# Kernel tuning notes

Hardware: AMD Instinct MI355X
Metric: run time of the kernel (lower is better)

The kernel has to match this reference:

```python
import jax, jax.numpy as jnp
import numpy as np

N = 32768      # total nodes
B = 64         # graphs
NPG = 512      # nodes per graph
E = 524288     # edges (avg degree 16)
H = 4          # heads
Fh = 64        # per-head dim
C = H * Fh     # 256
FIN = 128
RATIO = 0.5


def gat(x, src, dst, W, a_src, a_dst, bias, n_nodes):
    # PyG GATConv: linear -> add self-loops -> edge softmax over dst -> scatter-add
    h = (x @ W).reshape(n_nodes, H, Fh)
    loop = jnp.arange(n_nodes)
    s = jnp.concatenate([src, loop])
    d = jnp.concatenate([dst, loop])
    es = jnp.sum(h * a_src, axis=-1)  # [N,H]
    ed = jnp.sum(h * a_dst, axis=-1)  # [N,H]
    e = jax.nn.leaky_relu(es[s] + ed[d], 0.2)  # [E+N,H]
    m = jax.ops.segment_max(e, d, num_segments=n_nodes)
    ex = jnp.exp(e - m[d])
    den = jax.ops.segment_sum(ex, d, num_segments=n_nodes)
    alpha = ex / (den[d] + 1e-16)  # [E+N,H]
    out = jax.ops.segment_sum(alpha[:, :, None] * h[s], d, num_segments=n_nodes)
    return out.reshape(n_nodes, C) + bias


def pool(x, sw, sb, tw, tb, n_graphs, n_per):
    # equal-size graphs -> per-graph top-k as a batched top_k
    k = max(1, int(n_per * RATIO))
    scores = jax.nn.sigmoid(x @ sw + sb)[:, 0].reshape(n_graphs, n_per)
    _, idx = jax.lax.top_k(scores, k)  # [B,k]
    xb = x.reshape(n_graphs, n_per, x.shape[-1])
    sel = jnp.take_along_axis(xb, idx[:, :, None], axis=1)
    sel = sel.reshape(n_graphs * k, x.shape[-1])
    return sel @ tw + tb, k


def setup_inputs() -> dict:
    key = jax.random.key(0)
    ks = jax.random.split(key, 24)
    x = jax.random.normal(ks[0], (N, FIN), dtype=jnp.float32)
    # within-graph random edges
    gbase = jnp.repeat(jnp.arange(B, dtype=jnp.int32) * NPG, E // B)
    src = gbase + jax.random.randint(ks[1], (E,), 0, NPG)
    dst = gbase + jax.random.randint(ks[2], (E,), 0, NPG)
    edge_index = jnp.stack([src, dst]).astype(jnp.int32)
    batch = jnp.repeat(jnp.arange(B, dtype=jnp.int32), NPG)
    def lin(k, fi, fo):
        return jax.random.normal(k, (fi, fo), dtype=jnp.float32) / np.sqrt(fi)
    inp = dict(x=x, edge_index=edge_index, batch=batch)
    inp["W1"] = lin(ks[3], FIN, C)
    inp["a_src1"] = jax.random.normal(ks[4], (H, Fh), jnp.float32) / np.sqrt(Fh)
    inp["a_dst1"] = jax.random.normal(ks[5], (H, Fh), jnp.float32) / np.sqrt(Fh)
    inp["b1"] = jnp.zeros((C,), jnp.float32)
    inp["W2"] = lin(ks[6], C, C)
    inp["a_src2"] = jax.random.normal(ks[7], (H, Fh), jnp.float32) / np.sqrt(Fh)
    inp["a_dst2"] = jax.random.normal(ks[8], (H, Fh), jnp.float32) / np.sqrt(Fh)
    inp["b2"] = jnp.zeros((C,), jnp.float32)
    inp["p1_sw"] = lin(ks[9], C, 1)
    inp["p1_sb"] = jnp.zeros((1,), jnp.float32)
    inp["p1_tw"] = lin(ks[10], C, C)
    inp["p1_tb"] = jnp.zeros((C,), jnp.float32)
    inp["p2_sw"] = lin(ks[11], C, 1)
    inp["p2_sb"] = jnp.zeros((1,), jnp.float32)
    inp["p2_tw"] = lin(ks[12], C, C)
    inp["p2_tb"] = jnp.zeros((C,), jnp.float32)
    inp["c1w"] = lin(ks[13], C, 64)
    inp["c1b"] = jnp.zeros((64,), jnp.float32)
    inp["c2w"] = lin(ks[14], 64, 2)
    inp["c2b"] = jnp.zeros((2,), jnp.float32)
    return inp


def reference(x, edge_index, batch, W1, a_src1, a_dst1, b1, W2, a_src2, a_dst2, b2,
              p1_sw, p1_sb, p1_tw, p1_tb, p2_sw, p2_sb, p2_tw, p2_tb,
              c1w, c1b, c2w, c2b):
    src, dst = edge_index[0], edge_index[1]
    h = jax.nn.elu(gat(x, src, dst, W1, a_src1, a_dst1, b1, N))
    h = jax.nn.elu(gat(h, src, dst, W2, a_src2, a_dst2, b2, N))
    # pool1 then pool2 (edge_index after pooling is never consumed by the output path)
    h, k1 = pool(h, p1_sw, p1_sb, p1_tw, p1_tb, B, NPG)
    h, k2 = pool(h, p2_sw, p2_sb, p2_tw, p2_tb, B, k1)
    g = h.reshape(B, k2, C).mean(axis=1)  # global mean pool per graph
    g = jax.nn.relu(g @ c1w + c1b)
    g = g @ c2w + c2b
    return jax.nn.log_softmax(g, axis=1)
```

## Files before the change

kernel.cpp:

```cpp
#include <hip/hip_runtime.h>
#include <hip/hip_bf16.h>
#include <hip/hip_fp16.h>
#include <math.h>

constexpr int NN  = 32768;
constexpr int BG  = 64;
constexpr int NPG = 512;
constexpr int EG  = 524288;
constexpr int EPG = EG / BG;
constexpr int HH  = 4;
constexpr int FH  = 64;
constexpr int CC  = 256;
constexpr int FIN = 128;
constexpr int KP1 = 256;
constexpr int KP2 = 128;
constexpr int NS  = 4;

typedef __attribute__((ext_vector_type(8))) short short8;
typedef __attribute__((ext_vector_type(4))) float f32x4;
typedef __attribute__((ext_vector_type(2))) float f32x2v;

__device__ inline float leaky02(float v) { return v > 0.0f ? v : 0.2f * v; }

__device__ inline unsigned short f2bf(float v) {
    __hip_bfloat16 h = __float2bfloat16(v);
    return *(unsigned short*)&h;
}
__device__ inline float bf2f(unsigned short u) {
    __hip_bfloat16 h;
    *(unsigned short*)&h = u;
    return __bfloat162float(h);
}
__device__ inline void split2(float v, unsigned short& hi, unsigned short& lo) {
    hi = f2bf(v);
    lo = f2bf(v - bf2f(hi));
}
__device__ inline void split8(const float* p, short8& hi, short8& lo) {
    const float4 f0 = *(const float4*)p;
    const float4 f1 = *(const float4*)(p + 4);
    unsigned short h, l;
    split2(f0.x, h, l); hi[0] = (short)h; lo[0] = (short)l;
    split2(f0.y, h, l); hi[1] = (short)h; lo[1] = (short)l;
    split2(f0.z, h, l); hi[2] = (short)h; lo[2] = (short)l;
    split2(f0.w, h, l); hi[3] = (short)h; lo[3] = (short)l;
    split2(f1.x, h, l); hi[4] = (short)h; lo[4] = (short)l;
    split2(f1.y, h, l); hi[5] = (short)h; lo[5] = (short)l;
    split2(f1.z, h, l); hi[6] = (short)h; lo[6] = (short)l;
    split2(f1.w, h, l); hi[7] = (short)h; lo[7] = (short)l;
}

__device__ inline unsigned short f2h(float v) {
    __half h = __float2half(v);
    return *(unsigned short*)&h;
}

__device__ inline unsigned int fmap(float v) {
    unsigned int b = __float_as_uint(v);
    return (b & 0x80000000u) ? ~b : (b | 0x80000000u);
}

__device__ inline void acc8h(const unsigned short* p, float a, f32x2v* acc) {
    const uint4 u = *(const uint4*)p;
    const __half2* hp = (const __half2*)&u;
    f32x2v av; av[0] = a; av[1] = a;
#pragma unroll
    for (int i = 0; i < 4; ++i) {
        const float2 f = __half22float2(hp[i]);
        f32x2v fv; fv[0] = f.x; fv[1] = f.y;
        acc[i] = __builtin_elementwise_fma(fv, av, acc[i]);
    }
}

__global__ __launch_bounds__(1024) void setup_k(
        const int* __restrict__ src, const int* __restrict__ dst,
        int* __restrict__ rowp, int* __restrict__ esrc,
        const float* __restrict__ tw1, const float* __restrict__ sw2,
        const float* __restrict__ tb1, const float* __restrict__ sb2,
        float* __restrict__ w12, float* __restrict__ b12,
        const float* __restrict__ tw2, const float* __restrict__ c1w,
        const float* __restrict__ tb2, float* __restrict__ T,
        float* __restrict__ bc2,
        const float* __restrict__ W1, const float* __restrict__ W2,
        unsigned short* __restrict__ w1ph, unsigned short* __restrict__ w1pl,
        unsigned short* __restrict__ w2ph, unsigned short* __restrict__ w2pl) {
    __shared__ int lcnt[NPG];
    __shared__ int wsum[8];
    const int b = blockIdx.x;
    const int t = threadIdx.x;
    if (b < BG) {
        const int g = b;
        const int ebase = g * EPG;
        const int nbase = g * NPG;
        if (t < NPG) lcnt[t] = 0;
        __syncthreads();
        int ds[EPG / 1024];
#pragma unroll
        for (int j = 0; j < EPG / 1024; ++j) {
            ds[j] = dst[ebase + t + 1024 * j] - nbase;
            atomicAdd(&lcnt[ds[j]], 1);
        }
        __syncthreads();
        int c = 0, sInc = 0;
        if (t < NPG) {
            c = lcnt[t];
            sInc = c;
#pragma unroll
            for (int o = 1; o < 64; o <<= 1) {
                int v = __shfl_up(sInc, o);
                if ((t & 63) >= o) sInc += v;
            }
            if ((t & 63) == 63) wsum[t >> 6] = sInc;
        }
        __syncthreads();
        if (t < 8) {
            int v = wsum[t];
            int s = v;
#pragma unroll
            for (int o = 1; o < 8; o <<= 1) {
                int u2 = __shfl_up(s, o, 8);
                if (t >= o) s += u2;
            }
            wsum[t] = s - v;
        }
        __syncthreads();
        if (t < NPG) {
            const int ex = sInc - c + wsum[t >> 6];
            rowp[nbase + t] = ebase + ex;
            lcnt[t] = ex;
        }
        if (g == BG - 1 && t == 0) rowp[NN] = EG;
        __syncthreads();
#pragma unroll
        for (int j = 0; j < EPG / 1024; ++j) {
            int p = atomicAdd(&lcnt[ds[j]], 1);
            esrc[ebase + p] = src[ebase + t + 1024 * j];
        }
        return;
    }
    if (t >= 256) return;
    const int pb = b - BG;
    if (pb < 66) {
        if (pb == 0) {
            float s = 0.0f;
            for (int o = 0; o < CC; ++o) s += tw1[t * CC + o] * sw2[o];
            w12[t] = s;
            if (t == 0) {
                float bb = 0.0f;
                for (int o = 0; o < CC; ++o) bb += tb1[o] * sw2[o];
                *b12 = bb + sb2[0];
            }
        } else if (pb < 65) {
            const int r = (pb - 1) * 4 + (t >> 6);
            const int cth = t & 63;
            float s = 0.0f;
            for (int j = 0; j < CC; ++j) s = fmaf(tw2[r * CC + j], c1w[j * 64 + cth], s);
            T[r * 64 + cth] = s;
        } else if (t < 64) {
            float s = 0.0f;
            for (int j = 0; j < CC; ++j) s = fmaf(tb2[j], c1w[j * 64 + t], s);
            bc2[t] = s;
        }
    } else {
        const int idx = (pb - 66) * 256 + t;
        if (idx < 4096) {
            const int nt = idx >> 8, rem = idx & 255;
            const int kg = rem >> 6, l = rem & 63;
            const int n = nt * 16 + (l & 15);
            const int kb = kg * 32 + (l >> 4) * 8;
            unsigned short h[8], lo[8];
#pragma unroll
            for (int j = 0; j < 8; ++j) split2(W1[(kb + j) * CC + n], h[j], lo[j]);
#pragma unroll
            for (int j = 0; j < 8; ++j) {
                w1ph[(size_t)idx * 8 + j] = h[j];
                w1pl[(size_t)idx * 8 + j] = lo[j];
            }
        } else {
            const int i2 = idx - 4096;
            const int nt = i2 >> 9, rem = i2 & 511;
            const int kg = rem >> 6, l = rem & 63;
            const int n = nt * 16 + (l & 15);
            const int kb = kg * 32 + (l >> 4) * 8;
            unsigned short h[8], lo[8];
#pragma unroll
            for (int j = 0; j < 8; ++j) split2(W2[(kb + j) * CC + n], h[j], lo[j]);
#pragma unroll
            for (int j = 0; j < 8; ++j) {
                w2ph[(size_t)i2 * 8 + j] = h[j];
                w2pl[(size_t)i2 * 8 + j] = lo[j];
            }
        }
    }
}

__global__ __launch_bounds__(256, 4) void gemm_mfma_attn(
        const unsigned short* __restrict__ Ahi, const unsigned short* __restrict__ Alo,
        const unsigned short* __restrict__ Bph, const unsigned short* __restrict__ Bpl,
        unsigned short* __restrict__ Cb, int K,
        const float* __restrict__ a_src, const float* __restrict__ a_dst,
        float* __restrict__ es, float* __restrict__ ed) {
    const int t = threadIdx.x;
    const int w = t >> 6;
    const int l = t & 63;
    const int bx   = blockIdx.x;
    const int xcd  = bx & 7;
    const int slot = bx >> 3;
    const int gph  = xcd + ((slot >> 4) << 3);
    const int row0 = gph * NPG + ((slot & 15) << 5);
    const int m = l & 15;
    const int q = l >> 4;
    const int ncol0 = w * 64;
    const int KG = K >> 5;

    const unsigned short* aH0 = Ahi + (size_t)(row0 + m) * K + q * 8;
    const unsigned short* aL0 = Alo + (size_t)(row0 + m) * K + q * 8;
    const unsigned short* aH1 = aH0 + (size_t)16 * K;
    const unsigned short* aL1 = aL0 + (size_t)16 * K;

    f32x4 acc0[4], acc1[4];
#pragma unroll
    for (int c = 0; c < 4; ++c) {
        acc0[c] = (f32x4){0.f, 0.f, 0.f, 0.f};
        acc1[c] = (f32x4){0.f, 0.f, 0.f, 0.f};
    }

    for (int kg = 0; kg < KG; ++kg) {
        const int ko = kg * 32;
        short8 ah0 = *(const short8*)(aH0 + ko);
        short8 al0 = *(const short8*)(aL0 + ko);
        short8 ah1 = *(const short8*)(aH1 + ko);
        short8 al1 = *(const short8*)(aL1 + ko);
#pragma unroll
        for (int c = 0; c < 4; ++c) {
            const int nt = (w << 2) + c;
            const size_t boff = ((size_t)(nt * KG + kg) * 64 + l) * 8;
            short8 bh = *(const short8*)(Bph + boff);
            short8 bl = *(const short8*)(Bpl + boff);
            acc0[c] = __builtin_amdgcn_mfma_f32_16x16x32_bf16(ah0, bh, acc0[c], 0, 0, 0);
            acc0[c] = __builtin_amdgcn_mfma_f32_16x16x32_bf16(ah0, bl, acc0[c], 0, 0, 0);
            acc0[c] = __builtin_amdgcn_mfma_f32_16x16x32_bf16(al0, bh, acc0[c], 0, 0, 0);
            acc1[c] = __builtin_amdgcn_mfma_f32_16x16x32_bf16(ah1, bh, acc1[c], 0, 0, 0);
            acc1[c] = __builtin_amdgcn_mfma_f32_16x16x32_bf16(ah1, bl, acc1[c], 0, 0, 0);
            acc1[c] = __builtin_amdgcn_mfma_f32_16x16x32_bf16(al1, bh, acc1[c], 0, 0, 0);
        }
    }

#pragma unroll
    for (int c = 0; c < 4; ++c)
#pragma unroll
        for (int r = 0; r < 4; ++r) {
            Cb[(size_t)(row0 + q * 4 + r) * CC + ncol0 + c * 16 + m] = f2h(acc0[c][r]);
            Cb[(size_t)(row0 + 16 + q * 4 + r) * CC + ncol0 + c * 16 + m] = f2h(acc1[c][r]);
        }

    float asv[4], adv[4];
#pragma unroll
    for (int c = 0; c < 4; ++c) {
        asv[c] = a_src[ncol0 + c * 16 + m];
        adv[c] = a_dst[ncol0 + c * 16 + m];
    }
#pragma unroll
    for (int r = 0; r < 4; ++r) {
        float ps0 = 0.f, pd0 = 0.f, ps1 = 0.f, pd1 = 0.f;
#pragma unroll
        for (int c = 0; c < 4; ++c) {
            ps0 = fmaf(acc0[c][r], asv[c], ps0);
            pd0 = fmaf(acc0[c][r], adv[c], pd0);
            ps1 = fmaf(acc1[c][r], asv[c], ps1);
            pd1 = fmaf(acc1[c][r], adv[c], pd1);
        }
#pragma unroll
        for (int o = 8; o >= 1; o >>= 1) {
            ps0 += __shfl_down(ps0, o, 16);
            pd0 += __shfl_down(pd0, o, 16);
            ps1 += __shfl_down(ps1, o, 16);
            pd1 += __shfl_down(pd1, o, 16);
        }
        if (m == 0) {
            es[(row0 + q * 4 + r) * HH + w] = ps0;
            ed[(row0 + q * 4 + r) * HH + w] = pd0;
            es[(row0 + 16 + q * 4 + r) * HH + w] = ps1;
            ed[(row0 + 16 + q * 4 + r) * HH + w] = pd1;
        }
    }
}

__global__ __launch_bounds__(256, 4) void gemm_mfma_attn_f32(
        const float* __restrict__ Af,
        const unsigned short* __restrict__ Bph, const unsigned short* __restrict__ Bpl,
        unsigned short* __restrict__ Cb, int K,
        const float* __restrict__ a_src, const float* __restrict__ a_dst,
        float* __restrict__ es, float* __restrict__ ed,
        const float* __restrict__ tw1, const float* __restrict__ T,
        const float* __restrict__ tb1, const float* __restrict__ bc2,
        const float* __restrict__ c1b, float* __restrict__ Wc,
        float* __restrict__ bcv) {
    const int t = threadIdx.x;
    const int bx = blockIdx.x;
    if (bx >= NN / 32) {
        const int fb = bx - NN / 32;
        if (fb < 64) {
            const int r = fb * 4 + (t >> 6);
            const int cth = t & 63;
            float s = 0.0f;
            for (int j = 0; j < CC; ++j) s = fmaf(tw1[r * CC + j], T[j * 64 + cth], s);
            Wc[r * 64 + cth] = s;
        } else if (t < 64) {
            float s = 0.0f;
            for (int j = 0; j < CC; ++j) s = fmaf(tb1[j], T[j * 64 + t], s);
            bcv[t] = s + bc2[t] + c1b[t];
        }
        return;
    }
    const int w = t >> 6;
    const int l = t & 63;
    const int xcd  = bx & 7;
    const int slot = bx >> 3;
    const int gph  = xcd + ((slot >> 4) << 3);
    const int row0 = gph * NPG + ((slot & 15) << 5);
    const int m = l & 15;
    const int q = l >> 4;
    const int ncol0 = w * 64;
    const int KG = K >> 5;

    const float* aF0 = Af + (size_t)(row0 + m) * K + q * 8;
    const float* aF1 = aF0 + (size_t)16 * K;

    f32x4 acc0[4], acc1[4];
#pragma unroll
    for (int c = 0; c < 4; ++c) {
        acc0[c] = (f32x4){0.f, 0.f, 0.f, 0.f};
        acc1[c] = (f32x4){0.f, 0.f, 0.f, 0.f};
    }

    for (int kg = 0; kg < KG; ++kg) {
        const int ko = kg * 32;
        short8 ah0, al0, ah1, al1;
        split8(aF0 + ko, ah0, al0);
        split8(aF1 + ko, ah1, al1);
#pragma unroll
        for (int c = 0; c < 4; ++c) {
            const int nt = (w << 2) + c;
            const size_t boff = ((size_t)(nt * KG + kg) * 64 + l) * 8;
            short8 bh = *(const short8*)(Bph + boff);
            short8 bl = *(const short8*)(Bpl + boff);
            acc0[c] = __builtin_amdgcn_mfma_f32_16x16x32_bf16(ah0, bh, acc0[c], 0, 0, 0);
            acc0[c] = __builtin_amdgcn_mfma_f32_16x16x32_bf16(ah0, bl, acc0[c], 0, 0, 0);
            acc0[c] = __builtin_amdgcn_mfma_f32_16x16x32_bf16(al0, bh, acc0[c], 0, 0, 0);
            acc1[c] = __builtin_amdgcn_mfma_f32_16x16x32_bf16(ah1, bh, acc1[c], 0, 0, 0);
            acc1[c] = __builtin_amdgcn_mfma_f32_16x16x32_bf16(ah1, bl, acc1[c], 0, 0, 0);
            acc1[c] = __builtin_amdgcn_mfma_f32_16x16x32_bf16(al1, bh, acc1[c], 0, 0, 0);
        }
    }

#pragma unroll
    for (int c = 0; c < 4; ++c)
#pragma unroll
        for (int r = 0; r < 4; ++r) {
            Cb[(size_t)(row0 + q * 4 + r) * CC + ncol0 + c * 16 + m] = f2h(acc0[c][r]);
            Cb[(size_t)(row0 + 16 + q * 4 + r) * CC + ncol0 + c * 16 + m] = f2h(acc1[c][r]);
        }

    float asv[4], adv[4];
#pragma unroll
    for (int c = 0; c < 4; ++c) {
        asv[c] = a_src[ncol0 + c * 16 + m];
        adv[c] = a_dst[ncol0 + c * 16 + m];
    }
#pragma unroll
    for (int r = 0; r < 4; ++r) {
        float ps0 = 0.f, pd0 = 0.f, ps1 = 0.f, pd1 = 0.f;
#pragma unroll
        for (int c = 0; c < 4; ++c) {
            ps0 = fmaf(acc0[c][r], asv[c], ps0);
            pd0 = fmaf(acc0[c][r], adv[c], pd0);
            ps1 = fmaf(acc1[c][r], asv[c], ps1);
            pd1 = fmaf(acc1[c][r], adv[c], pd1);
        }
#pragma unroll
        for (int o = 8; o >= 1; o >>= 1) {
            ps0 += __shfl_down(ps0, o, 16);
            pd0 += __shfl_down(pd0, o, 16);
            ps1 += __shfl_down(ps1, o, 16);
            pd1 += __shfl_down(pd1, o, 16);
        }
        if (m == 0) {
            es[(row0 + q * 4 + r) * HH + w] = ps0;
            ed[(row0 + q * 4 + r) * HH + w] = pd0;
            es[(row0 + 16 + q * 4 + r) * HH + w] = ps1;
            ed[(row0 + 16 + q * 4 + r) * HH + w] = pd1;
        }
    }
}

__global__ __launch_bounds__(256) void gat_edge(const unsigned short* __restrict__ zh,
                                                const int* __restrict__ rowp,
                                                const int* __restrict__ esrc,
                                                const float* __restrict__ es,
                                                const float* __restrict__ ed,
                                                const float* __restrict__ bias,
                                                float* __restrict__ out,
                                                unsigned short* __restrict__ outh,
                                                unsigned short* __restrict__ outl,
                                                const float* __restrict__ sw1,
                                                const float* __restrict__ sb1,
                                                const float* __restrict__ w12,
                                                const float* __restrict__ b12,
                                                float* __restrict__ sc1,
                                                float* __restrict__ sc2) {
    const int w = threadIdx.x >> 6;
    const int l = threadIdx.x & 63;
    const int b    = blockIdx.x;
    const int xcd  = b & 7;
    const int slot = b >> 3;
    const int gph  = xcd + ((slot >> 7) << 3);
    const int d    = gph * NPG + ((slot & 127) << 2) + w;

    const int h    = l & 3;
    const int ei   = l >> 2;
    const int lh   = l & 31;
    const int half = l >> 5;
    const int hcol = lh >> 3;
    const int c0   = lh << 3;

    const int beg = rowp[d];
    const int deg = rowp[d + 1] - beg;

    f32x2v acc[4];
#pragma unroll
    for (int i = 0; i < 4; ++i) acc[i] = (f32x2v){0.f, 0.f};

    if (deg <= 16 * NS) {
        const float edh = ed[d * HH + h];
        int   sidx[NS];
        float v[NS];
#pragma unroll
        for (int j = 0; j < NS; ++j) { sidx[j] = d; v[j] = 0.0f; }
        float vmax = -INFINITY, eself = 0.0f, vself = 0.0f;
        if (ei == 0) {
            vself = leaky02(es[d * HH + h] + edh);
            vmax = vself;
        }
#pragma unroll
        for (int j = 0; j < NS; ++j) {
            int i = ei + 16 * j;
            if (i < deg) {
                sidx[j] = esrc[beg + i];
                v[j] = leaky02(es[sidx[j] * HH + h] + edh);
                vmax = fmaxf(vmax, v[j]);
            }
        }
#pragma unroll
        for (int o = 4; o <= 32; o <<= 1) vmax = fmaxf(vmax, __shfl_xor(vmax, o));
        float dsum = 0.0f;
#pragma unroll
        for (int j = 0; j < NS; ++j) {
            int i = ei + 16 * j;
            if (i < deg) { v[j] = __expf(v[j] - vmax); dsum += v[j]; }
        }
        if (ei == 0) { eself = __expf(vself - vmax); dsum += eself; }
#pragma unroll
        for (int o = 4; o <= 32; o <<= 1) dsum += __shfl_xor(dsum, o);
        const float inv = 1.0f / (dsum + 1e-16f);
#pragma unroll
        for (int j = 0; j < NS; ++j) v[j] *= inv;
        eself *= inv;

        float aself = __shfl(eself, hcol);
        if (half) aself = 0.0f;
        acc8h(zh + (size_t)d * CC + c0, aself, acc);

#pragma unroll
        for (int j = 0; j < NS; ++j) {
            if (16 * j < deg) {
#pragma unroll
                for (int rr = 0; rr < 8; ++rr) {
                    if (16 * j + 2 * rr < deg) {
                        const int slb  = (2 * rr + half) << 2;
                        const int srcn = __shfl(sidx[j], slb);
                        const float a  = __shfl(v[j], slb + hcol);
                        acc8h(zh + (size_t)srcn * CC + c0, a, acc);
                    }
                }
            }
        }
    } else {
        const float edh = ed[d * HH + h];
        float vmax = (ei == 0) ? leaky02(es[d * HH + h] + edh) : -INFINITY;
        for (int i = ei; i < deg; i += 16)
            vmax = fmaxf(vmax, leaky02(es[esrc[beg + i] * HH + h] + edh));
#pragma unroll
        for (int o = 4; o <= 32; o <<= 1) vmax = fmaxf(vmax, __shfl_xor(vmax, o));
        float dsum = (ei == 0) ? __expf(leaky02(es[d * HH + h] + edh) - vmax) : 0.0f;
        for (int i = ei; i < deg; i += 16)
            dsum += __expf(leaky02(es[esrc[beg + i] * HH + h] + edh) - vmax);
#pragma unroll
        for (int o = 4; o <= 32; o <<= 1) dsum += __shfl_xor(dsum, o);
        const float inv = 1.0f / (dsum + 1e-16f);

        const float vmaxc = __shfl(vmax, hcol);
        const float invc  = __shfl(inv,  hcol);
        const float edh4  = ed[d * HH + hcol];
        float a0 = __expf(leaky02(es[d * HH + hcol] + edh4) - vmaxc) * invc;
        if (half) a0 = 0.0f;
        acc8h(zh + (size_t)d * CC + c0, a0, acc);
        for (int e = half; e < deg; e += 2) {
            const int srcn = esrc[beg + e];
            const float a = __expf(leaky02(es[srcn * HH + hcol] + edh4) - vmaxc) * invc;
            acc8h(zh + (size_t)srcn * CC + c0, a, acc);
        }
    }

#pragma unroll
    for (int i = 0; i < 4; ++i) {
        float a0 = acc[i][0]; a0 += __shfl_xor(a0, 32);
        float a1 = acc[i][1]; a1 += __shfl_xor(a1, 32);
        acc[i][0] = a0; acc[i][1] = a1;
    }

    const int cw = c0 + (half << 2);
    float o0 = half ? acc[2][0] : acc[0][0];
    float o1 = half ? acc[2][1] : acc[0][1];
    float o2 = half ? acc[3][0] : acc[1][0];
    float o3 = half ? acc[3][1] : acc[1][1];

    const float4 bv = *(const float4*)(bias + cw);
    o0 += bv.x; o0 = o0 > 0.0f ? o0 : __expf(o0) - 1.0f;
    o1 += bv.y; o1 = o1 > 0.0f ? o1 : __expf(o1) - 1.0f;
    o2 += bv.z; o2 = o2 > 0.0f ? o2 : __expf(o2) - 1.0f;
    o3 += bv.w; o3 = o3 > 0.0f ? o3 : __expf(o3) - 1.0f;

    if (out) *(float4*)(out + (size_t)d * CC + cw) = make_float4(o0, o1, o2, o3);
    if (outh) {
        ushort4 uh, ul;
        split2(o0, uh.x, ul.x);
        split2(o1, uh.y, ul.y);
        split2(o2, uh.z, ul.z);
        split2(o3, uh.w, ul.w);
        *(ushort4*)(outh + (size_t)d * CC + cw) = uh;
        *(ushort4*)(outl + (size_t)d * CC + cw) = ul;
    }

    if (sc1) {
        const float4 s1 = *(const float4*)(sw1 + cw);
        const float4 s2 = *(const float4*)(w12 + cw);
        float r1 = o0 * s1.x + o1 * s1.y + o2 * s1.z + o3 * s1.w;
        float r2 = o0 * s2.x + o1 * s2.y + o2 * s2.z + o3 * s2.w;
#pragma unroll
        for (int off = 32; off >= 1; off >>= 1) {
            r1 += __shfl_xor(r1, off);
            r2 += __shfl_xor(r2, off);
        }
        if (l == 0) {
            sc1[d] = r1 + sb1[0];
            sc2[d] = r2 + b12[0];
        }
    }
}

__global__ __launch_bounds__(512) void pool_g(const float* __restrict__ sc1,
                                              const float* __restrict__ sc2,
                                              const float* __restrict__ feat,
                                              const float* __restrict__ Wc,
                                              const float* __restrict__ bc,
                                              const float* __restrict__ c2w,
                                              const float* __restrict__ c2b,
                                              float* __restrict__ outp) {
    __shared__ unsigned int us[NPG];
    __shared__ unsigned char kb[NPG];
    __shared__ int list[KP2];
    __shared__ float v0[CC];
    __shared__ float vbuf[2][CC];
    __shared__ float part[4][64];
    __shared__ float v2[64];
    const int g = blockIdx.x;
    const int t = threadIdx.x;
    const int lane = t & 63, wid = t >> 6;

    const float s2val = sc2[(size_t)g * NPG + t];
    us[t] = fmap(sc1[(size_t)g * NPG + t]);
    __syncthreads();

    if (wid == 0) {
        unsigned int u[8];
#pragma unroll
        for (int j = 0; j < 8; ++j) u[j] = us[j * 64 + lane];
        unsigned int p = 0;
        for (int bb = 31; bb >= 0; --bb) {
            const unsigned int cand = p | (1u << bb);
            int cnt = 0;
#pragma unroll
            for (int j = 0; j < 8; ++j) cnt += __popcll(__ballot(u[j] >= cand));
            if (cnt >= KP1) p = cand;
        }
        int cgt = 0;
#pragma unroll
        for (int j = 0; j < 8; ++j) cgt += __popcll(__ballot(u[j] > p));
        const int kk = KP1 - cgt;
        const unsigned long long lm = (1ull << lane) - 1ull;
        int preEq = 0;
#pragma unroll
        for (int j = 0; j < 8; ++j) {
            const unsigned long long balEq = __ballot(u[j] == p);
            const int eqr = preEq + __popcll(balEq & lm);
            preEq += __popcll(balEq);
            kb[j * 64 + lane] =
                (unsigned char)((u[j] > p) || ((u[j] == p) && (eqr < kk)));
        }
    }
    __syncthreads();

    us[t] = kb[t] ? fmap(s2val) : 0u;
    __syncthreads();
    if (wid == 0) {
        unsigned int u[8];
#pragma unroll
        for (int j = 0; j < 8; ++j) u[j] = us[j * 64 + lane];
        unsigned int p = 0;
        for (int bb = 31; bb >= 0; --bb) {
            const unsigned int cand = p | (1u << bb);
            int cnt = 0;
#pragma unroll
            for (int j = 0; j < 8; ++j) cnt += __popcll(__ballot(u[j] >= cand));
            if (cnt >= KP2) p = cand;
        }
        int cgt = 0;
#pragma unroll
        for (int j = 0; j < 8; ++j) cgt += __popcll(__ballot(u[j] > p));
        const int kk = KP2 - cgt;
        const unsigned long long lm = (1ull << lane) - 1ull;
        int preEq = 0, preKeep = 0;
#pragma unroll
        for (int j = 0; j < 8; ++j) {
            const unsigned long long balEq = __ballot(u[j] == p);
            const int eqr = preEq + __popcll(balEq & lm);
            preEq += __popcll(balEq);
            const int keep = (u[j] > p) || ((u[j] == p) && (eqr < kk));
            const unsigned long long balK = __ballot(keep);
            const int pos = preKeep + __popcll(balK & lm);
            preKeep += __popcll(balK);
            if (keep) list[pos] = j * 64 + lane;
        }
    }
    __syncthreads();

    {
        const int col = t & (CC - 1);
        const int hf = t >> 8;
        float acc = 0.0f;
        for (int i = hf * 64; i < hf * 64 + 64; ++i)
            acc += feat[((size_t)g * NPG + list[i]) * CC + col];
        vbuf[hf][col] = acc;
    }
    __syncthreads();
    if (t < CC) v0[t] = (vbuf[0][t] + vbuf[1][t]) * (1.0f / KP2);
    __syncthreads();

    if (t < 256) {
        const int q = t >> 6, cth = t & 63;
        float pr = 0.0f;
        for (int j = q * 64; j < q * 64 + 64; ++j)
            pr = fmaf(v0[j], Wc[j * 64 + cth], pr);
        part[q][cth] = pr;
    }
    __syncthreads();
    if (t < 64) {
        float u = bc[t];
#pragma unroll
        for (int q = 0; q < 4; ++q) u += part[q][t];
        v2[t] = fmaxf(u, 0.0f);
    }
    __syncthreads();
    if (t < 2) {
        float o = c2b[t];
        for (int j = 0; j < 64; ++j) o = fmaf(v2[j], c2w[j * 2 + t], o);
        part[0][t] = o;
    }
    __syncthreads();
    if (t == 0) {
        float a = part[0][0], bq = part[0][1];
        float mx = fmaxf(a, bq);
        float lse = mx + logf(expf(a - mx) + expf(bq - mx));
        outp[g * 2 + 0] = a - lse;
        outp[g * 2 + 1] = bq - lse;
    }
}

extern "C" void kernel_launch(void* const* d_in, const int* in_sizes, int n_in,
                              void* d_out, int out_size, void* d_ws, size_t ws_size,
                              hipStream_t stream) {
    const float* x      = (const float*)d_in[0];
    const int*   ei     = (const int*)d_in[1];
    const int*   src    = ei;
    const int*   dst    = ei + EG;
    const float* W1     = (const float*)d_in[3];
    const float* a_src1 = (const float*)d_in[4];
    const float* a_dst1 = (const float*)d_in[5];
    const float* b1     = (const float*)d_in[6];
    const float* W2     = (const float*)d_in[7];
    const float* a_src2 = (const float*)d_in[8];
    const float* a_dst2 = (const float*)d_in[9];
    const float* b2     = (const float*)d_in[10];
    const float* p1_sw  = (const float*)d_in[11];
    const float* p1_sb  = (const float*)d_in[12];
    const float* p1_tw  = (const float*)d_in[13];
    const float* p1_tb  = (const float*)d_in[14];
    const float* p2_sw  = (const float*)d_in[15];
    const float* p2_sb  = (const float*)d_in[16];
    const float* p2_tw  = (const float*)d_in[17];
    const float* p2_tb  = (const float*)d_in[18];
    const float* c1w    = (const float*)d_in[19];
    const float* c1b    = (const float*)d_in[20];
    const float* c2w    = (const float*)d_in[21];
    const float* c2b    = (const float*)d_in[22];
    float* out = (float*)d_out;

    float* ws = (float*)d_ws;
    float* z = ws;
    unsigned short* zh = (unsigned short*)z;
    float* fregion = z + (size_t)NN * CC;
    unsigned short* fhi = (unsigned short*)fregion;
    unsigned short* flo = fhi + (size_t)NN * CC;
    float* featF = fregion;
    float* wsp = fregion + (size_t)NN * CC;
    unsigned short* w1ph = (unsigned short*)wsp;
    unsigned short* w1pl = w1ph + 256 * FIN;
    unsigned short* w2ph = w1pl + 256 * FIN;
    unsigned short* w2pl = w2ph + 256 * CC;
    float* es  = (float*)(w2pl + 256 * CC);
    float* ed  = es + NN * HH;
    int* rowp  = (int*)(ed + NN * HH);
    int* esrc  = rowp + NN + 1;
    float* sc1 = (float*)(esrc + EG);
    float* sc2 = sc1 + NN;
    int* sel1  = (int*)(sc2 + NN);
    float* w12 = (float*)(sel1 + NN);
    float* b12 = w12 + CC;
    float* T   = b12 + 64;
    float* Wc  = T + CC * 64;
    float* bc2 = Wc + CC * 64;
    float* bcv = bc2 + 64;

    setup_k<<<BG + 66 + 48, 1024, 0, stream>>>(
        src, dst, rowp, esrc,
        p1_tw, p2_sw, p1_tb, p2_sb, w12, b12, p2_tw, c1w, p2_tb, T, bc2,
        W1, W2, w1ph, w1pl, w2ph, w2pl);

    gemm_mfma_attn_f32<<<NN / 32 + 65, 256, 0, stream>>>(
        x, w1ph, w1pl, zh, FIN, a_src1, a_dst1, es, ed,
        p1_tw, T, p1_tb, bc2, c1b, Wc, bcv);
    gat_edge<<<NN / 4, 256, 0, stream>>>(zh, rowp, esrc, es, ed, b1,
                                         nullptr, fhi, flo,
                                         nullptr, nullptr, nullptr, nullptr,
                                         nullptr, nullptr);

    gemm_mfma_attn<<<NN / 32, 256, 0, stream>>>(fhi, flo, w2ph, w2pl, zh, CC,
                                                a_src2, a_dst2, es, ed);
    gat_edge<<<NN / 4, 256, 0, stream>>>(zh, rowp, esrc, es, ed, b2,
                                         featF, nullptr, nullptr,
                                         p1_sw, p1_sb, w12, b12, sc1, sc2);

    pool_g<<<BG, 512, 0, stream>>>(sc1, sc2, featF, Wc, bcv, c2w, c2b, out);
}
```

Baseline: 258.6 us.

## Fuse first GAT edge aggregation with second-layer GEMM through shared memory

The first-layer edge softmax/aggregation is merged with the second-layer MFMA GEMM into one kernel. Each block aggregates 32 destination rows, stores the split hi/lo bf16 features in swizzled LDS, then runs the GEMM and attention-logit reduction from LDS. This removes the global write and reload of the hi/lo intermediate feature matrices and one kernel launch. In exchange, the edge phase now runs with fewer blocks (32 rows per block instead of 4), which lowers parallelism for the gather. It also uses 32KB of LDS per block and needs separate zh2/es2/ed2 buffers.

Result: faster. 243.4 us (-5.9%).

```diff
diff --git a/kernel.cpp b/kernel.cpp
--- a/kernel.cpp
+++ b/kernel.cpp
@@ -189,98 +189,6 @@
                 w2ph[(size_t)i2 * 8 + j] = h[j];
                 w2pl[(size_t)i2 * 8 + j] = lo[j];
             }
-        }
-    }
-}
-
-__global__ __launch_bounds__(256, 4) void gemm_mfma_attn(
-        const unsigned short* __restrict__ Ahi, const unsigned short* __restrict__ Alo,
-        const unsigned short* __restrict__ Bph, const unsigned short* __restrict__ Bpl,
-        unsigned short* __restrict__ Cb, int K,
-        const float* __restrict__ a_src, const float* __restrict__ a_dst,
-        float* __restrict__ es, float* __restrict__ ed) {
-    const int t = threadIdx.x;
-    const int w = t >> 6;
-    const int l = t & 63;
-    const int bx   = blockIdx.x;
-    const int xcd  = bx & 7;
-    const int slot = bx >> 3;
-    const int gph  = xcd + ((slot >> 4) << 3);
-    const int row0 = gph * NPG + ((slot & 15) << 5);
-    const int m = l & 15;
-    const int q = l >> 4;
-    const int ncol0 = w * 64;
-    const int KG = K >> 5;
-
-    const unsigned short* aH0 = Ahi + (size_t)(row0 + m) * K + q * 8;
-    const unsigned short* aL0 = Alo + (size_t)(row0 + m) * K + q * 8;
-    const unsigned short* aH1 = aH0 + (size_t)16 * K;
-    const unsigned short* aL1 = aL0 + (size_t)16 * K;
-
-    f32x4 acc0[4], acc1[4];
-#pragma unroll
-    for (int c = 0; c < 4; ++c) {
-        acc0[c] = (f32x4){0.f, 0.f, 0.f, 0.f};
-        acc1[c] = (f32x4){0.f, 0.f, 0.f, 0.f};
-    }
-
-    for (int kg = 0; kg < KG; ++kg) {
-        const int ko = kg * 32;
-        short8 ah0 = *(const short8*)(aH0 + ko);
-        short8 al0 = *(const short8*)(aL0 + ko);
-        short8 ah1 = *(const short8*)(aH1 + ko);
-        short8 al1 = *(const short8*)(aL1 + ko);
-#pragma unroll
-        for (int c = 0; c < 4; ++c) {
-            const int nt = (w << 2) + c;
-            const size_t boff = ((size_t)(nt * KG + kg) * 64 + l) * 8;
-            short8 bh = *(const short8*)(Bph + boff);
-            short8 bl = *(const short8*)(Bpl + boff);
-            acc0[c] = __builtin_amdgcn_mfma_f32_16x16x32_bf16(ah0, bh, acc0[c], 0, 0, 0);
-            acc0[c] = __builtin_amdgcn_mfma_f32_16x16x32_bf16(ah0, bl, acc0[c], 0, 0, 0);
-            acc0[c] = __builtin_amdgcn_mfma_f32_16x16x32_bf16(al0, bh, acc0[c], 0, 0, 0);
-            acc1[c] = __builtin_amdgcn_mfma_f32_16x16x32_bf16(ah1, bh, acc1[c], 0, 0, 0);
-            acc1[c] = __builtin_amdgcn_mfma_f32_16x16x32_bf16(ah1, bl, acc1[c], 0, 0, 0);
-            acc1[c] = __builtin_amdgcn_mfma_f32_16x16x32_bf16(al1, bh, acc1[c], 0, 0, 0);
-        }
-    }
-
-#pragma unroll
-    for (int c = 0; c < 4; ++c)
-#pragma unroll
-        for (int r = 0; r < 4; ++r) {
-            Cb[(size_t)(row0 + q * 4 + r) * CC + ncol0 + c * 16 + m] = f2h(acc0[c][r]);
-            Cb[(size_t)(row0 + 16 + q * 4 + r) * CC + ncol0 + c * 16 + m] = f2h(acc1[c][r]);
-        }
-
-    float asv[4], adv[4];
-#pragma unroll
-    for (int c = 0; c < 4; ++c) {
-        asv[c] = a_src[ncol0 + c * 16 + m];
-        adv[c] = a_dst[ncol0 + c * 16 + m];
-    }
-#pragma unroll
-    for (int r = 0; r < 4; ++r) {
-        float ps0 = 0.f, pd0 = 0.f, ps1 = 0.f, pd1 = 0.f;
-#pragma unroll
-        for (int c = 0; c < 4; ++c) {
-            ps0 = fmaf(acc0[c][r], asv[c], ps0);
-            pd0 = fmaf(acc0[c][r], adv[c], pd0);
-            ps1 = fmaf(acc1[c][r], asv[c], ps1);
-            pd1 = fmaf(acc1[c][r], adv[c], pd1);
-        }
-#pragma unroll
-        for (int o = 8; o >= 1; o >>= 1) {
-            ps0 += __shfl_down(ps0, o, 16);
-            pd0 += __shfl_down(pd0, o, 16);
-            ps1 += __shfl_down(ps1, o, 16);
-            pd1 += __shfl_down(pd1, o, 16);
-        }
-        if (m == 0) {
-            es[(row0 + q * 4 + r) * HH + w] = ps0;
-            ed[(row0 + q * 4 + r) * HH + w] = pd0;
-            es[(row0 + 16 + q * 4 + r) * HH + w] = ps1;
-            ed[(row0 + 16 + q * 4 + r) * HH + w] = pd1;
         }
     }
 }
@@ -393,6 +301,230 @@
     }
 }
 
+__global__ __launch_bounds__(256) void edge1_gemm2(
+        const unsigned short* __restrict__ zh1,
+        const int* __restrict__ rowp, const int* __restrict__ esrc,
+        const float* __restrict__ es1, const float* __restrict__ ed1,
+        const float* __restrict__ bias,
+        const unsigned short* __restrict__ Bph, const unsigned short* __restrict__ Bpl,
+        unsigned short* __restrict__ zh2,
+        const float* __restrict__ a_src, const float* __restrict__ a_dst,
+        float* __restrict__ es2, float* __restrict__ ed2) {
+    __shared__ unsigned char AhB[32 * 512];
+    __shared__ unsigned char AlB[32 * 512];
+    const int t = threadIdx.x;
+    const int w = t >> 6;
+    const int l = t & 63;
+    const int bx   = blockIdx.x;
+    const int xcd  = bx & 7;
+    const int slot = bx >> 3;
+    const int gph  = xcd + ((slot >> 4) << 3);
+    const int row0 = gph * NPG + ((slot & 15) << 5);
+
+    const int h    = l & 3;
+    const int ei   = l >> 2;
+    const int lh   = l & 31;
+    const int half = l >> 5;
+    const int hcol = lh >> 3;
+    const int c0   = lh << 3;
+
+    for (int nd = 0; nd < 8; ++nd) {
+        const int rloc = w * 8 + nd;
+        const int d = row0 + rloc;
+        const int beg = rowp[d];
+        const int deg = rowp[d + 1] - beg;
+
+        f32x2v acc[4];
+#pragma unroll
+        for (int i = 0; i < 4; ++i) acc[i] = (f32x2v){0.f, 0.f};
+
+        if (deg <= 16 * NS) {
+            const float edh = ed1[d * HH + h];
+            int   sidx[NS];
+            float v[NS];
+#pragma unroll
+            for (int j = 0; j < NS; ++j) { sidx[j] = d; v[j] = 0.0f; }
+            float vmax = -INFINITY, eself = 0.0f, vself = 0.0f;
+            if (ei == 0) {
+                vself = leaky02(es1[d * HH + h] + edh);
+                vmax = vself;
+            }
+#pragma unroll
+            for (int j = 0; j < NS; ++j) {
+                int i = ei + 16 * j;
+                if (i < deg) {
+                    sidx[j] = esrc[beg + i];
+                    v[j] = leaky02(es1[sidx[j] * HH + h] + edh);
+                    vmax = fmaxf(vmax, v[j]);
+                }
+            }
+#pragma unroll
+            for (int o = 4; o <= 32; o <<= 1) vmax = fmaxf(vmax, __shfl_xor(vmax, o));
+            float dsum = 0.0f;
+#pragma unroll
+            for (int j = 0; j < NS; ++j) {
+                int i = ei + 16 * j;
+                if (i < deg) { v[j] = __expf(v[j] - vmax); dsum += v[j]; }
+            }
+            if (ei == 0) { eself = __expf(vself - vmax); dsum += eself; }
+#pragma unroll
+            for (int o = 4; o <= 32; o <<= 1) dsum += __shfl_xor(dsum, o);
+            const float inv = 1.0f / (dsum + 1e-16f);
+#pragma unroll
+            for (int j = 0; j < NS; ++j) v[j] *= inv;
+            eself *= inv;
+
+            float aself = __shfl(eself, hcol);
+            if (half) aself = 0.0f;
+            acc8h(zh1 + (size_t)d * CC + c0, aself, acc);
+
+#pragma unroll
+            for (int j = 0; j < NS; ++j) {
+                if (16 * j < deg) {
+#pragma unroll
+                    for (int rr = 0; rr < 8; ++rr) {
+                        if (16 * j + 2 * rr < deg) {
+                            const int slb  = (2 * rr + half) << 2;
+                            const int srcn = __shfl(sidx[j], slb);
+                            const float a  = __shfl(v[j], slb + hcol);
+                            acc8h(zh1 + (size_t)srcn * CC + c0, a, acc);
+                        }
+                    }
+                }
+            }
+        } else {
+            const float edh = ed1[d * HH + h];
+            float vmax = (ei == 0) ? leaky02(es1[d * HH + h] + edh) : -INFINITY;
+            for (int i = ei; i < deg; i += 16)
+                vmax = fmaxf(vmax, leaky02(es1[esrc[beg + i] * HH + h] + edh));
+#pragma unroll
+            for (int o = 4; o <= 32; o <<= 1) vmax = fmaxf(vmax, __shfl_xor(vmax, o));
+            float dsum = (ei == 0) ? __expf(leaky02(es1[d * HH + h] + edh) - vmax) : 0.0f;
+            for (int i = ei; i < deg; i += 16)
+                dsum += __expf(leaky02(es1[esrc[beg + i] * HH + h] + edh) - vmax);
+#pragma unroll
+            for (int o = 4; o <= 32; o <<= 1) dsum += __shfl_xor(dsum, o);
+            const float inv = 1.0f / (dsum + 1e-16f);
+
+            const float vmaxc = __shfl(vmax, hcol);
+            const float invc  = __shfl(inv,  hcol);
+            const float edh4  = ed1[d * HH + hcol];
+            float a0 = __expf(leaky02(es1[d * HH + hcol] + edh4) - vmaxc) * invc;
+            if (half) a0 = 0.0f;
+            acc8h(zh1 + (size_t)d * CC + c0, a0, acc);
+            for (int e = half; e < deg; e += 2) {
+                const int srcn = esrc[beg + e];
+                const float a = __expf(leaky02(es1[srcn * HH + hcol] + edh4) - vmaxc) * invc;
+                acc8h(zh1 + (size_t)srcn * CC + c0, a, acc);
+            }
+        }
+
+#pragma unroll
+        for (int i = 0; i < 4; ++i) {
+            float a0 = acc[i][0]; a0 += __shfl_xor(a0, 32);
+            float a1 = acc[i][1]; a1 += __shfl_xor(a1, 32);
+            acc[i][0] = a0; acc[i][1] = a1;
+        }
+
+        const int cw = c0 + (half << 2);
+        float o0 = half ? acc[2][0] : acc[0][0];
+        float o1 = half ? acc[2][1] : acc[0][1];
+        float o2 = half ? acc[3][0] : acc[1][0];
+        float o3 = half ? acc[3][1] : acc[1][1];
+
+        const float4 bv = *(const float4*)(bias + cw);
+        o0 += bv.x; o0 = o0 > 0.0f ? o0 : __expf(o0) - 1.0f;
+        o1 += bv.y; o1 = o1 > 0.0f ? o1 : __expf(o1) - 1.0f;
+        o2 += bv.z; o2 = o2 > 0.0f ? o2 : __expf(o2) - 1.0f;
+        o3 += bv.w; o3 = o3 > 0.0f ? o3 : __expf(o3) - 1.0f;
+
+        ushort4 uh, ul;
+        split2(o0, uh.x, ul.x);
+        split2(o1, uh.y, ul.y);
+        split2(o2, uh.z, ul.z);
+        split2(o3, uh.w, ul.w);
+        const size_t bo = (size_t)(((rloc * 512) + cw * 2) ^ ((rloc & 7) << 4));
+        *(ushort4*)(AhB + bo) = uh;
+        *(ushort4*)(AlB + bo) = ul;
+    }
+
+    __syncthreads();
+
+    const int m = l & 15;
+    const int q = l >> 4;
+    const int ncol0 = w * 64;
+    constexpr int KG = CC >> 5;
+
+    f32x4 acc0[4], acc1[4];
+#pragma unroll
+    for (int c = 0; c < 4; ++c) {
+        acc0[c] = (f32x4){0.f, 0.f, 0.f, 0.f};
+        acc1[c] = (f32x4){0.f, 0.f, 0.f, 0.f};
+    }
+
+    for (int kg = 0; kg < KG; ++kg) {
+        const int co = kg * 64 + q * 16;
+        const size_t bo0 = (size_t)(((m * 512) + co) ^ ((m & 7) << 4));
+        const size_t bo1 = (size_t)((((16 + m) * 512) + co) ^ ((m & 7) << 4));
+        short8 ah0 = *(const short8*)(AhB + bo0);
+        short8 al0 = *(const short8*)(AlB + bo0);
+        short8 ah1 = *(const short8*)(AhB + bo1);
+        short8 al1 = *(const short8*)(AlB + bo1);
+#pragma unroll
+        for (int c = 0; c < 4; ++c) {
+            const int nt = (w << 2) + c;
+            const size_t boff = ((size_t)(nt * KG + kg) * 64 + l) * 8;
+            short8 bh = *(const short8*)(Bph + boff);
+            short8 bl = *(const short8*)(Bpl + boff);
+            acc0[c] = __builtin_amdgcn_mfma_f32_16x16x32_bf16(ah0, bh, acc0[c], 0, 0, 0);
+            acc0[c] = __builtin_amdgcn_mfma_f32_16x16x32_bf16(ah0, bl, acc0[c], 0, 0, 0);
+            acc0[c] = __builtin_amdgcn_mfma_f32_16x16x32_bf16(al0, bh, acc0[c], 0, 0, 0);
+            acc1[c] = __builtin_amdgcn_mfma_f32_16x16x32_bf16(ah1, bh, acc1[c], 0, 0, 0);
+            acc1[c] = __builtin_amdgcn_mfma_f32_16x16x32_bf16(ah1, bl, acc1[c], 0, 0, 0);
+            acc1[c] = __builtin_amdgcn_mfma_f32_16x16x32_bf16(al1, bh, acc1[c], 0, 0, 0);
+        }
+    }
+
+#pragma unroll
+    for (int c = 0; c < 4; ++c)
+#pragma unroll
+        for (int r = 0; r < 4; ++r) {
+            zh2[(size_t)(row0 + q * 4 + r) * CC + ncol0 + c * 16 + m] = f2h(acc0[c][r]);
+            zh2[(size_t)(row0 + 16 + q * 4 + r) * CC + ncol0 + c * 16 + m] = f2h(acc1[c][r]);
+        }
+
+    float asv[4], adv[4];
+#pragma unroll
+    for (int c = 0; c < 4; ++c) {
+        asv[c] = a_src[ncol0 + c * 16 + m];
+        adv[c] = a_dst[ncol0 + c * 16 + m];
+    }
+#pragma unroll
+    for (int r = 0; r < 4; ++r) {
+        float ps0 = 0.f, pd0 = 0.f, ps1 = 0.f, pd1 = 0.f;
+#pragma unroll
+        for (int c = 0; c < 4; ++c) {
+            ps0 = fmaf(acc0[c][r], asv[c], ps0);
+            pd0 = fmaf(acc0[c][r], adv[c], pd0);
+            ps1 = fmaf(acc1[c][r], asv[c], ps1);
+            pd1 = fmaf(acc1[c][r], adv[c], pd1);
+        }
+#pragma unroll
+        for (int o = 8; o >= 1; o >>= 1) {
+            ps0 += __shfl_down(ps0, o, 16);
+            pd0 += __shfl_down(pd0, o, 16);
+            ps1 += __shfl_down(ps1, o, 16);
+            pd1 += __shfl_down(pd1, o, 16);
+        }
+        if (m == 0) {
+            es2[(row0 + q * 4 + r) * HH + w] = ps0;
+            ed2[(row0 + q * 4 + r) * HH + w] = pd0;
+            es2[(row0 + 16 + q * 4 + r) * HH + w] = ps1;
+            ed2[(row0 + 16 + q * 4 + r) * HH + w] = pd1;
+        }
+    }
+}
+
 __global__ __launch_bounds__(256) void gat_edge(const unsigned short* __restrict__ zh,
                                                 const int* __restrict__ rowp,
                                                 const int* __restrict__ esrc,
@@ -400,8 +532,6 @@
                                                 const float* __restrict__ ed,
                                                 const float* __restrict__ bias,
                                                 float* __restrict__ out,
-                                                unsigned short* __restrict__ outh,
-                                                unsigned short* __restrict__ outl,
                                                 const float* __restrict__ sw1,
                                                 const float* __restrict__ sb1,
                                                 const float* __restrict__ w12,
@@ -530,18 +660,9 @@
     o2 += bv.z; o2 = o2 > 0.0f ? o2 : __expf(o2) - 1.0f;
     o3 += bv.w; o3 = o3 > 0.0f ? o3 : __expf(o3) - 1.0f;
 
-    if (out) *(float4*)(out + (size_t)d * CC + cw) = make_float4(o0, o1, o2, o3);
-    if (outh) {
-        ushort4 uh, ul;
-        split2(o0, uh.x, ul.x);
-        split2(o1, uh.y, ul.y);
-        split2(o2, uh.z, ul.z);
-        split2(o3, uh.w, ul.w);
-        *(ushort4*)(outh + (size_t)d * CC + cw) = uh;
-        *(ushort4*)(outl + (size_t)d * CC + cw) = ul;
-    }
-
-    if (sc1) {
+    *(float4*)(out + (size_t)d * CC + cw) = make_float4(o0, o1, o2, o3);
+
+    {
         const float4 s1 = *(const float4*)(sw1 + cw);
         const float4 s2 = *(const float4*)(w12 + cw);
         float r1 = o0 * s1.x + o1 * s1.y + o2 * s1.z + o3 * s1.w;
@@ -717,10 +838,9 @@
 
     float* ws = (float*)d_ws;
     float* z = ws;
-    unsigned short* zh = (unsigned short*)z;
+    unsigned short* zh1 = (unsigned short*)z;
+    unsigned short* zh2 = zh1 + (size_t)NN * CC;
     float* fregion = z + (size_t)NN * CC;
-    unsigned short* fhi = (unsigned short*)fregion;
-    unsigned short* flo = fhi + (size_t)NN * CC;
     float* featF = fregion;
     float* wsp = fregion + (size_t)NN * CC;
     unsigned short* w1ph = (unsigned short*)wsp;
@@ -740,6 +860,8 @@
     float* Wc  = T + CC * 64;
     float* bc2 = Wc + CC * 64;
     float* bcv = bc2 + 64;
+    float* es2 = bcv + 64;
+    float* ed2 = es2 + (size_t)NN * HH;
 
     setup_k<<<BG + 66 + 48, 1024, 0, stream>>>(
         src, dst, rowp, esrc,
@@ -747,18 +869,16 @@
         W1, W2, w1ph, w1pl, w2ph, w2pl);
 
     gemm_mfma_attn_f32<<<NN / 32 + 65, 256, 0, stream>>>(
-        x, w1ph, w1pl, zh, FIN, a_src1, a_dst1, es, ed,
+        x, w1ph, w1pl, zh1, FIN, a_src1, a_dst1, es, ed,
         p1_tw, T, p1_tb, bc2, c1b, Wc, bcv);
-    gat_edge<<<NN / 4, 256, 0, stream>>>(zh, rowp, esrc, es, ed, b1,
-                                         nullptr, fhi, flo,
-                                         nullptr, nullptr, nullptr, nullptr,
-                                         nullptr, nullptr);
-
-    gemm_mfma_attn<<<NN / 32, 256, 0, stream>>>(fhi, flo, w2ph, w2pl, zh, CC,
-                                                a_src2, a_dst2, es, ed);
-    gat_edge<<<NN / 4, 256, 0, stream>>>(zh, rowp, esrc, es, ed, b2,
-                                         featF, nullptr, nullptr,
-                                         p1_sw, p1_sb, w12, b12, sc1, sc2);
+
+    edge1_gemm2<<<NN / 32, 256, 0, stream>>>(
+        zh1, rowp, esrc, es, ed, b1,
+        w2ph, w2pl, zh2, a_src2, a_dst2, es2, ed2);
+
+    gat_edge<<<NN / 4, 256, 0, stream>>>(zh2, rowp, esrc, es2, ed2, b2,
+                                         featF, p1_sw, p1_sb, w12, b12,
+                                         sc1, sc2);
 
     pool_g<<<BG, 512, 0, stream>>>(sc1, sc2, featF, Wc, bcv, c2w, c2b, out);
 }
```
